# Performance work log

Hardware: AMD Instinct MI355X
Metric: run time of the kernel (lower is better)

The kernel has to match this reference:

```python
import jax, jax.numpy as jnp
import numpy as np

B, NQ, NKV, D = 16, 256, 256, 64


def setup_inputs() -> dict:
    key = jax.random.key(0)
    k1, k2, k3, k4, k5 = jax.random.split(key, 5)
    return {
        "v_equi": jax.random.normal(k1, (B, NKV, 3, D), dtype=jnp.float32),
        "messages": jax.random.normal(k2, (B, NQ, NKV, D), dtype=jnp.float32),
        "adj_mask": jax.random.randint(k3, (B, NQ, NKV), 0, 2, dtype=jnp.int32),
        "W_coord": jax.random.normal(k4, (D, D), dtype=jnp.float32) / np.sqrt(D),
        "W_attn": jax.random.normal(k5, (D, D), dtype=jnp.float32) / np.sqrt(D),
    }


def reference(v_equi, messages, adj_mask, W_coord, W_attn):
    adj = adj_mask.astype(bool)                              # [B,Nq,Nkv]
    # adj_to_attn_mask: -inf where no edge, but rows with no edges at all -> 0
    mask = jnp.where(adj, 0.0, -jnp.inf).astype(jnp.float32)
    row_empty = ~jnp.any(adj, axis=-1)                       # [B,Nq]
    mask = jnp.where(row_empty[..., None], 0.0, mask)
    # coord_proj (Linear, no bias): y = x @ W^T over last dim
    proj_equi = v_equi @ W_coord.T                           # [B,Nkv,3,D]
    # masked softmax over N_kv (dim=2), per equi channel d
    attn = jax.nn.softmax(messages + mask[..., None], axis=2)  # [B,Nq,Nkv,D]
    # batched skinny bmm over (B, d): [Nq,Nkv] @ [Nkv,3]
    attn_out = jnp.einsum("bqkd,bkcd->bqcd", attn, proj_equi)  # [B,Nq,3,D]
    # L2 norm of attention rows as a scale
    weights = jnp.sqrt(jnp.sum(attn * attn, axis=2))           # [B,Nq,D]
    attn_out = attn_out * weights[:, :, None, :]
    # attn_proj
    return attn_out @ W_attn.T                                 # [B,Nq,3,D]
```

## Files before the change

### kernel.cpp

```cpp
#include <hip/hip_runtime.h>
#include <math.h>

#define B_   16
#define NQ_  256
#define NKV_ 256
#define D_   64

__global__ __launch_bounds__(256) void proj_kernel(
    const float* __restrict__ v_equi, const float* __restrict__ W_coord,
    float* __restrict__ proj)
{
    __shared__ float WcT[64 * 65];
    __shared__ float vrow[4][64];

    int tid = threadIdx.x;
    for (int i = tid; i < 4096; i += 256) {
        int dd = i >> 6, e = i & 63;
        WcT[e * 65 + dd] = W_coord[i];
    }
    int r = tid >> 6, d = tid & 63;
    long long row0 = (long long)blockIdx.x * 4;
    vrow[r][d] = v_equi[row0 * 64 + tid];
    __syncthreads();

    float acc = 0.f;
#pragma unroll
    for (int e = 0; e < 64; ++e)
        acc = fmaf(vrow[r][e], WcT[e * 65 + d], acc);
    proj[(row0 + r) * 64 + d] = acc;
}

__global__ __launch_bounds__(256) void attn_kernel(
    const float* __restrict__ messages, const int* __restrict__ adj,
    const float* __restrict__ proj, const float* __restrict__ W_attn,
    float* __restrict__ out)
{
    __shared__ float WaT[64 * 65];
    __shared__ int   sadj[NKV_];
    __shared__ float red[5][16 * 64];
    __shared__ float ao[3][64];
    __shared__ int   anyw[4];

    int tid = threadIdx.x;
    int bq  = blockIdx.x;

    for (int i = tid; i < 4096; i += 256) {
        int dd = i >> 6, e = i & 63;
        WaT[e * 65 + dd] = W_attn[i];
    }

    int a = adj[(size_t)bq * NKV_ + tid];
    sadj[tid] = a;
    unsigned long long bal = __ballot(a != 0);
    if ((tid & 63) == 0) anyw[tid >> 6] = (bal != 0ULL) ? 1 : 0;
    __syncthreads();
    bool row_empty = (anyw[0] | anyw[1] | anyw[2] | anyw[3]) == 0;

    int d4 = (tid & 15) << 2;
    int kg = tid >> 4;
    int dq = d4 >> 2;

    const float4* mbase = (const float4*)(messages + (size_t)bq * NKV_ * D_);
    const float4* pbase = (const float4*)(proj + (size_t)(bq >> 8) * NKV_ * 3 * D_);

    float4 S  = make_float4(0.f, 0.f, 0.f, 0.f);
    float4 SS = make_float4(0.f, 0.f, 0.f, 0.f);
    float4 D0 = make_float4(0.f, 0.f, 0.f, 0.f);
    float4 D1 = make_float4(0.f, 0.f, 0.f, 0.f);
    float4 D2 = make_float4(0.f, 0.f, 0.f, 0.f);

#pragma unroll 4
    for (int i = 0; i < 16; ++i) {
        int k = kg * 16 + i;
        float4 m = mbase[k * 16 + dq];
        bool ok = (sadj[k] != 0) || row_empty;
        float4 p;
        if (ok) {
            p.x = __expf(m.x); p.y = __expf(m.y);
            p.z = __expf(m.z); p.w = __expf(m.w);
        } else {
            p = make_float4(0.f, 0.f, 0.f, 0.f);
        }
        float4 p0 = pbase[k * 48 + dq];
        float4 p1 = pbase[k * 48 + 16 + dq];
        float4 p2 = pbase[k * 48 + 32 + dq];

        S.x += p.x;  S.y += p.y;  S.z += p.z;  S.w += p.w;
        SS.x = fmaf(p.x, p.x, SS.x); SS.y = fmaf(p.y, p.y, SS.y);
        SS.z = fmaf(p.z, p.z, SS.z); SS.w = fmaf(p.w, p.w, SS.w);
        D0.x = fmaf(p.x, p0.x, D0.x); D0.y = fmaf(p.y, p0.y, D0.y);
        D0.z = fmaf(p.z, p0.z, D0.z); D0.w = fmaf(p.w, p0.w, D0.w);
        D1.x = fmaf(p.x, p1.x, D1.x); D1.y = fmaf(p.y, p1.y, D1.y);
        D1.z = fmaf(p.z, p1.z, D1.z); D1.w = fmaf(p.w, p1.w, D1.w);
        D2.x = fmaf(p.x, p2.x, D2.x); D2.y = fmaf(p.y, p2.y, D2.y);
        D2.z = fmaf(p.z, p2.z, D2.z); D2.w = fmaf(p.w, p2.w, D2.w);
    }

    int base = kg * 64 + d4;
    *(float4*)&red[0][base] = S;
    *(float4*)&red[1][base] = SS;
    *(float4*)&red[2][base] = D0;
    *(float4*)&red[3][base] = D1;
    *(float4*)&red[4][base] = D2;
    __syncthreads();

    if (tid < 64) {
        float s = 0.f, ss = 0.f, e0 = 0.f, e1 = 0.f, e2 = 0.f;
#pragma unroll
        for (int g = 0; g < 16; ++g) {
            s  += red[0][g * 64 + tid];
            ss += red[1][g * 64 + tid];
            e0 += red[2][g * 64 + tid];
            e1 += red[3][g * 64 + tid];
            e2 += red[4][g * 64 + tid];
        }
        float inv = 1.f / s;
        float scale = sqrtf(ss) * inv * inv;
        ao[0][tid] = e0 * scale;
        ao[1][tid] = e1 * scale;
        ao[2][tid] = e2 * scale;
    }
    __syncthreads();

    if (tid < 192) {
        int c = tid >> 6, dd = tid & 63;
        float acc = 0.f;
#pragma unroll
        for (int e = 0; e < 64; ++e)
            acc = fmaf(ao[c][e], WaT[e * 65 + dd], acc);
        out[((size_t)bq * 3 + c) * 64 + dd] = acc;
    }
}

extern "C" void kernel_launch(void* const* d_in, const int* in_sizes, int n_in,
                              void* d_out, int out_size, void* d_ws, size_t ws_size,
                              hipStream_t stream) {
    const float* v_equi   = (const float*)d_in[0];
    const float* messages = (const float*)d_in[1];
    const int*   adj      = (const int*)d_in[2];
    const float* W_coord  = (const float*)d_in[3];
    const float* W_attn   = (const float*)d_in[4];
    float* out  = (float*)d_out;
    float* proj = (float*)d_ws;

    proj_kernel<<<(B_ * NKV_ * 3) / 4, 256, 0, stream>>>(v_equi, W_coord, proj);
    attn_kernel<<<B_ * NQ_, 256, 0, stream>>>(messages, adj, proj, W_attn, out);
}
```

Measured before the change: 399.3 us.

## Split output projection into separate kernel and shrink attention shared-memory reduction

Moves the W_attn projection out of the attention kernel into a third launch that reuses a generic row-matmul kernel, so each attention block no longer loads and transposes the 64x64 weight. Shared memory drops from about 37KB to about 6KB, and the kernel now declares a min-blocks hint of 4, both aimed at higher occupancy on the memory-bound messages stream. The cross-thread reduction now uses wave shuffles before a small shared buffer. The key loop is interleaved so adjacent lanes read adjacent rows, and masking becomes a branch-free multiply. The cost is an extra launch plus a round trip of the intermediate result through global memory.

```diff
diff --git a/kernel.cpp b/kernel.cpp
--- a/kernel.cpp
+++ b/kernel.cpp
@@ -6,59 +6,50 @@
 #define NKV_ 256
 #define D_   64
 
-__global__ __launch_bounds__(256) void proj_kernel(
-    const float* __restrict__ v_equi, const float* __restrict__ W_coord,
-    float* __restrict__ proj)
+__global__ __launch_bounds__(256) void rowmat_kernel(
+    const float* __restrict__ in, const float* __restrict__ W,
+    float* __restrict__ out)
 {
-    __shared__ float WcT[64 * 65];
+    __shared__ float WT[64 * 65];
     __shared__ float vrow[4][64];
 
     int tid = threadIdx.x;
-    for (int i = tid; i < 4096; i += 256) {
-        int dd = i >> 6, e = i & 63;
-        WcT[e * 65 + dd] = W_coord[i];
-    }
+    for (int i = tid; i < 4096; i += 256)
+        WT[(i & 63) * 65 + (i >> 6)] = W[i];
+
     int r = tid >> 6, d = tid & 63;
-    long long row0 = (long long)blockIdx.x * 4;
-    vrow[r][d] = v_equi[row0 * 64 + tid];
+    size_t row0 = (size_t)blockIdx.x * 4;
+    vrow[r][d] = in[row0 * 64 + tid];
     __syncthreads();
 
     float acc = 0.f;
 #pragma unroll
     for (int e = 0; e < 64; ++e)
-        acc = fmaf(vrow[r][e], WcT[e * 65 + d], acc);
-    proj[(row0 + r) * 64 + d] = acc;
+        acc = fmaf(vrow[r][e], WT[e * 65 + d], acc);
+    out[(row0 + r) * 64 + d] = acc;
 }
 
-__global__ __launch_bounds__(256) void attn_kernel(
+__global__ __launch_bounds__(256, 4) void attn_kernel(
     const float* __restrict__ messages, const int* __restrict__ adj,
-    const float* __restrict__ proj, const float* __restrict__ W_attn,
-    float* __restrict__ out)
+    const float* __restrict__ proj, float* __restrict__ aout)
 {
-    __shared__ float WaT[64 * 65];
+    __shared__ float red[4][5][64];
     __shared__ int   sadj[NKV_];
-    __shared__ float red[5][16 * 64];
-    __shared__ float ao[3][64];
     __shared__ int   anyw[4];
 
-    int tid = threadIdx.x;
-    int bq  = blockIdx.x;
-
-    for (int i = tid; i < 4096; i += 256) {
-        int dd = i >> 6, e = i & 63;
-        WaT[e * 65 + dd] = W_attn[i];
-    }
+    int tid  = threadIdx.x;
+    int bq   = blockIdx.x;
+    int lane = tid & 63, w = tid >> 6;
 
     int a = adj[(size_t)bq * NKV_ + tid];
     sadj[tid] = a;
     unsigned long long bal = __ballot(a != 0);
-    if ((tid & 63) == 0) anyw[tid >> 6] = (bal != 0ULL) ? 1 : 0;
+    if (lane == 0) anyw[w] = (bal != 0ULL) ? 1 : 0;
     __syncthreads();
     bool row_empty = (anyw[0] | anyw[1] | anyw[2] | anyw[3]) == 0;
 
-    int d4 = (tid & 15) << 2;
+    int dq = tid & 15;
     int kg = tid >> 4;
-    int dq = d4 >> 2;
 
     const float4* mbase = (const float4*)(messages + (size_t)bq * NKV_ * D_);
     const float4* pbase = (const float4*)(proj + (size_t)(bq >> 8) * NKV_ * 3 * D_);
@@ -71,16 +62,13 @@
 
 #pragma unroll 4
     for (int i = 0; i < 16; ++i) {
-        int k = kg * 16 + i;
+        int k = i * 16 + kg;
         float4 m = mbase[k * 16 + dq];
-        bool ok = (sadj[k] != 0) || row_empty;
+        float wm = (sadj[k] != 0 || row_empty) ? 1.f : 0.f;
         float4 p;
-        if (ok) {
-            p.x = __expf(m.x); p.y = __expf(m.y);
-            p.z = __expf(m.z); p.w = __expf(m.w);
-        } else {
-            p = make_float4(0.f, 0.f, 0.f, 0.f);
-        }
+        p.x = __expf(m.x) * wm; p.y = __expf(m.y) * wm;
+        p.z = __expf(m.z) * wm; p.w = __expf(m.w) * wm;
+
         float4 p0 = pbase[k * 48 + dq];
         float4 p1 = pbase[k * 48 + 16 + dq];
         float4 p2 = pbase[k * 48 + 32 + dq];
@@ -96,39 +84,39 @@
         D2.z = fmaf(p.z, p2.z, D2.z); D2.w = fmaf(p.w, p2.w, D2.w);
     }
 
-    int base = kg * 64 + d4;
-    *(float4*)&red[0][base] = S;
-    *(float4*)&red[1][base] = SS;
-    *(float4*)&red[2][base] = D0;
-    *(float4*)&red[3][base] = D1;
-    *(float4*)&red[4][base] = D2;
+    float vals[20] = { S.x, S.y, S.z, S.w,  SS.x, SS.y, SS.z, SS.w,
+                       D0.x, D0.y, D0.z, D0.w, D1.x, D1.y, D1.z, D1.w,
+                       D2.x, D2.y, D2.z, D2.w };
+#pragma unroll
+    for (int j = 0; j < 20; ++j) {
+        vals[j] += __shfl_xor(vals[j], 16, 64);
+        vals[j] += __shfl_xor(vals[j], 32, 64);
+    }
+    if (lane < 16) {
+#pragma unroll
+        for (int q = 0; q < 5; ++q)
+            *(float4*)&red[w][q][dq * 4] =
+                make_float4(vals[q*4], vals[q*4+1], vals[q*4+2], vals[q*4+3]);
+    }
     __syncthreads();
 
     if (tid < 64) {
+        int d = tid;
         float s = 0.f, ss = 0.f, e0 = 0.f, e1 = 0.f, e2 = 0.f;
 #pragma unroll
-        for (int g = 0; g < 16; ++g) {
-            s  += red[0][g * 64 + tid];
-            ss += red[1][g * 64 + tid];
-            e0 += red[2][g * 64 + tid];
-            e1 += red[3][g * 64 + tid];
-            e2 += red[4][g * 64 + tid];
+        for (int w2 = 0; w2 < 4; ++w2) {
+            s  += red[w2][0][d];
+            ss += red[w2][1][d];
+            e0 += red[w2][2][d];
+            e1 += red[w2][3][d];
+            e2 += red[w2][4][d];
         }
         float inv = 1.f / s;
         float scale = sqrtf(ss) * inv * inv;
-        ao[0][tid] = e0 * scale;
-        ao[1][tid] = e1 * scale;
-        ao[2][tid] = e2 * scale;
-    }
-    __syncthreads();
-
-    if (tid < 192) {
-        int c = tid >> 6, dd = tid & 63;
-        float acc = 0.f;
-#pragma unroll
-        for (int e = 0; e < 64; ++e)
-            acc = fmaf(ao[c][e], WaT[e * 65 + dd], acc);
-        out[((size_t)bq * 3 + c) * 64 + dd] = acc;
+        float* ab = aout + (size_t)bq * 3 * 64;
+        ab[d]       = e0 * scale;
+        ab[64 + d]  = e1 * scale;
+        ab[128 + d] = e2 * scale;
     }
 }
 
@@ -141,8 +129,11 @@
     const float* W_coord  = (const float*)d_in[3];
     const float* W_attn   = (const float*)d_in[4];
     float* out  = (float*)d_out;
+
     float* proj = (float*)d_ws;
+    float* ao   = proj + (size_t)B_ * NKV_ * 3 * D_;
 
-    proj_kernel<<<(B_ * NKV_ * 3) / 4, 256, 0, stream>>>(v_equi, W_coord, proj);
-    attn_kernel<<<B_ * NQ_, 256, 0, stream>>>(messages, adj, proj, W_attn, out);
+    rowmat_kernel<<<(B_ * NKV_ * 3) / 4, 256, 0, stream>>>(v_equi, W_coord, proj);
+    attn_kernel<<<B_ * NQ_, 256, 0, stream>>>(messages, adj, proj, ao);
+    rowmat_kernel<<<(B_ * NQ_ * 3) / 4, 256, 0, stream>>>(ao, W_attn, out);
 }
```

Result: slower. 419.4 us (+5.1%).
